# Kernel tuning notes

Hardware: AMD Instinct MI355X
Metric: run time of the kernel (lower is better)

## Reference

```python
import jax, jax.numpy as jnp
import numpy as np

H = 16          # n_heads
DN = 128        # qk_nope_head_dim
DR = 64         # qk_rope_head_dim
DV = 128        # v_head_dim
R = 512         # kv_lora_rank
DIM = 2048
THETA = 10000.0
EPS = 1e-6
SCALE = (DN + DR) ** -0.5


def rms_norm(x, w):
    var = jnp.mean(x * x, axis=-1, keepdims=True)
    return x * jax.lax.rsqrt(var + EPS) * w


def rope_cos_sin(seqlen):
    # DeepSeek freqs: 1/theta^(2i/d) over adjacent pairs
    inv = 1.0 / (THETA ** (jnp.arange(0, DR, 2, dtype=jnp.float32) / DR))  # [DR/2]
    ang = jnp.arange(seqlen, dtype=jnp.float32)[:, None] * inv             # [s, DR/2]
    return jnp.cos(ang), jnp.sin(ang)


def apply_rope(t, cos, sin):
    # t: [b, s, h, DR]; rotate adjacent pairs (complex multiply)
    b, s, h, d = t.shape
    t = t.reshape(b, s, h, d // 2, 2)
    x0, x1 = t[..., 0], t[..., 1]
    c = cos[None, :, None, :]
    sn = sin[None, :, None, :]
    out = jnp.stack([x0 * c - x1 * sn, x0 * sn + x1 * c], axis=-1)
    return out.reshape(b, s, h, d)


def setup_inputs() -> dict:
    key = jax.random.key(0)
    ks = jax.random.split(key, 6)
    b, s = 2, 2048
    sc = lambda n: n ** -0.5
    return {
        "x": jax.random.normal(ks[0], (b, s, DIM), jnp.float32),
        "wq": jax.random.normal(ks[1], (DIM, H * (DN + DR)), jnp.float32) * sc(DIM),
        "wkv_a": jax.random.normal(ks[2], (DIM, R + DR), jnp.float32) * sc(DIM),
        "kv_norm_w": jnp.ones((R,), jnp.float32),
        "wkv_b": jax.random.normal(ks[3], (R, H * (DN + DV)), jnp.float32) * sc(R),
        "wo": jax.random.normal(ks[4], (H * DV, DIM), jnp.float32) * sc(H * DV),
    }


def reference(x, wq, wkv_a, kv_norm_w, wkv_b, wo):
    b, s, _ = x.shape
    cos, sin = rope_cos_sin(s)

    # Query projection (q_lora_rank == 0 -> direct)
    q = (x @ wq).reshape(b, s, H, DN + DR)
    q_nope, q_pe = q[..., :DN], q[..., DN:]
    q_pe = apply_rope(q_pe, cos, sin)

    # Compressed KV + decoupled rope key
    kv_a = x @ wkv_a                      # [b, s, R+DR]
    kv, k_pe = kv_a[..., :R], kv_a[..., R:]
    k_pe = apply_rope(k_pe[:, :, None, :], cos, sin)  # [b, s, 1, DR]
    kv = rms_norm(kv, kv_norm_w)
    kvb = (kv @ wkv_b).reshape(b, s, H, DN + DV)
    k_nope, v = kvb[..., :DN], kvb[..., DN:]

    qf = jnp.concatenate([q_nope, q_pe], axis=-1)                         # [b,s,H,192]
    kf = jnp.concatenate([k_nope, jnp.broadcast_to(k_pe, (b, s, H, DR))], axis=-1)

    scores = jnp.einsum("bshd,bthd->bhst", qf, kf) * SCALE
    mask = jnp.tril(jnp.ones((s, s), bool))
    scores = jnp.where(mask[None, None], scores, jnp.finfo(scores.dtype).min)
    p = jax.nn.softmax(scores, axis=-1)
    out = jnp.einsum("bhst,bthd->bshd", p, v).reshape(b, s, H * DV)
    return out @ wo
```

## Files before the change

kernel.cpp:

```cpp
#include <hip/hip_runtime.h>
#include <hip/hip_bf16.h>
#include <math.h>

#define NB 2
#define NS 2048
#define ND 2048
#define NH 16
#define DNOPE 128
#define DROPE 64
#define DVAL 128
#define RANK 512
#define QW (NH*(DNOPE+DROPE))
#define AW (RANK+DROPE)
#define AWPAD 640
#define BW (NH*(DNOPE+DVAL))
#define OW (NH*DVAL)
#define ATT_SCALE2 0.10411758590510176f
#define LOG2_10000 13.287712379549449f

typedef __attribute__((ext_vector_type(8))) short short8;
typedef __attribute__((ext_vector_type(4))) float f32x4;

__device__ __forceinline__ float b2f(unsigned short u) {
  unsigned x = ((unsigned)u) << 16; float f; __builtin_memcpy(&f, &x, 4); return f;
}
__device__ __forceinline__ unsigned short f2b(float f) {
  unsigned x; __builtin_memcpy(&x, &f, 4);
  unsigned r = (x + 0x7fffu + ((x >> 16) & 1u)) >> 16;
  return (unsigned short)r;
}
__device__ __forceinline__ unsigned cvtpk(float a, float b) {
  unsigned r;
  asm("v_cvt_pk_bf16_f32 %0, %1, %2" : "=v"(r) : "v"(a), "v"(b));
  return r;
}
__device__ __forceinline__ void gload16(const void* g, void* lds) {
  __builtin_amdgcn_global_load_lds((const __attribute__((address_space(1))) void*)g,
                                   (__attribute__((address_space(3))) void*)lds, 16, 0, 0);
}

__global__ __launch_bounds__(256) void k_cvt(const float* __restrict__ X,
                                             unsigned short* __restrict__ Y) {
  long i = ((long)blockIdx.x * 256 + threadIdx.x) * 4;
  float4 v = *(const float4*)(X + i);
  ushort4 o;
  o.x = f2b(v.x); o.y = f2b(v.y); o.z = f2b(v.z); o.w = f2b(v.w);
  *(ushort4*)(Y + i) = o;
}

__global__ __launch_bounds__(256) void k_transpose(const float* __restrict__ W,
                                                   unsigned short* __restrict__ WT,
                                                   int K, int N) {
  __shared__ float t[32][33];
  const int k0 = blockIdx.x * 32, n0 = blockIdx.y * 32;
  const int tx = threadIdx.x & 31, ty = threadIdx.x >> 5;
  #pragma unroll
  for (int i = 0; i < 32; i += 8) {
    int n = n0 + tx;
    float v = (n < N) ? W[(size_t)(k0 + ty + i) * N + n] : 0.f;
    t[ty + i][tx] = v;
  }
  __syncthreads();
  #pragma unroll
  for (int i = 0; i < 32; i += 8)
    WT[(size_t)(n0 + ty + i) * K + k0 + tx] = f2b(t[tx][ty + i]);
}

template <typename OutT>
__global__ __launch_bounds__(256) void gemm_bf16(
    const unsigned short* __restrict__ A, const unsigned short* __restrict__ BT,
    OutT* __restrict__ C, int M, int N, int K, int lda) {
  __shared__ short8 AsV[1024];
  __shared__ short8 BsV[1024];
  const int tid = threadIdx.x;
  const int l = tid & 63, w = tid >> 6;
  const int nwg = gridDim.x * gridDim.y;
  const int bid = blockIdx.y * gridDim.x + blockIdx.x;
  const int sbid = (bid & 7) * (nwg >> 3) + (bid >> 3);
  const int bx = sbid % gridDim.x, by = sbid / gridDim.x;
  const int bm = by * 128, bn = bx * 128;
  const int wm = (w >> 1) * 64, wn = (w & 1) * 64;
  f32x4 acc[4][4] = {};

  const int srow = tid >> 3;
  const int gk   = ((((tid & 7) * 16) ^ ((srow & 7) << 4)) >> 1);
  const int sw   = l & 7;

  for (int k0 = 0; k0 < K; k0 += 64) {
    #pragma unroll
    for (int i = 0; i < 4; ++i) {
      const int row = i * 32 + srow;
      gload16(A + (size_t)(bm + row) * lda + k0 + gk, (char*)AsV + i * 4096 + w * 1024);
      gload16(BT + (size_t)(bn + row) * K   + k0 + gk, (char*)BsV + i * 4096 + w * 1024);
    }
    __syncthreads();
    #pragma unroll
    for (int kk2 = 0; kk2 < 2; ++kk2) {
      const int kb = kk2 * 4 + (l >> 4);
      short8 af[4], bg[4];
      #pragma unroll
      for (int mi = 0; mi < 4; ++mi)
        af[mi] = AsV[(wm + mi * 16 + (l & 15)) * 8 + (kb ^ sw)];
      #pragma unroll
      for (int ni = 0; ni < 4; ++ni)
        bg[ni] = BsV[(wn + ni * 16 + (l & 15)) * 8 + (kb ^ sw)];
      #pragma unroll
      for (int mi = 0; mi < 4; ++mi)
        #pragma unroll
        for (int ni = 0; ni < 4; ++ni)
          acc[mi][ni] = __builtin_amdgcn_mfma_f32_16x16x32_bf16(af[mi], bg[ni], acc[mi][ni], 0, 0, 0);
    }
    __syncthreads();
  }

  const int r0 = bm + wm + (l >> 4) * 4;
  const int c0 = bn + wn + (l & 15);
  #pragma unroll
  for (int mi = 0; mi < 4; ++mi)
    #pragma unroll
    for (int ni = 0; ni < 4; ++ni) {
      const int col = c0 + ni * 16;
      if (col < N) {
        #pragma unroll
        for (int j = 0; j < 4; ++j) {
          float v = acc[mi][ni][j];
          if constexpr (__is_same(OutT, float))
            C[(size_t)(r0 + mi * 16 + j) * N + col] = v;
          else
            C[(size_t)(r0 + mi * 16 + j) * N + col] = f2b(v);
        }
      }
    }
}

__global__ __launch_bounds__(256) void gemm_fused_qkva(
    const unsigned short* __restrict__ A, const unsigned short* __restrict__ BT,
    unsigned short* __restrict__ Cq, unsigned short* __restrict__ Ckva, int K) {
  __shared__ short8 AsV[1024];
  __shared__ short8 BsV[1024];
  const int tid = threadIdx.x;
  const int l = tid & 63, w = tid >> 6;
  const int nwg = gridDim.x * gridDim.y;
  const int bid = blockIdx.y * gridDim.x + blockIdx.x;
  const int sbid = (bid & 7) * (nwg >> 3) + (bid >> 3);
  const int bx = sbid % gridDim.x, by = sbid / gridDim.x;
  const int bm = by * 128, bn = bx * 128;
  const int wm = (w >> 1) * 64, wn = (w & 1) * 64;
  f32x4 acc[4][4] = {};

  const int srow = tid >> 3;
  const int gk   = ((((tid & 7) * 16) ^ ((srow & 7) << 4)) >> 1);
  const int sw   = l & 7;

  for (int k0 = 0; k0 < K; k0 += 64) {
    #pragma unroll
    for (int i = 0; i < 4; ++i) {
      const int row = i * 32 + srow;
      gload16(A + (size_t)(bm + row) * K + k0 + gk, (char*)AsV + i * 4096 + w * 1024);
      gload16(BT + (size_t)(bn + row) * K + k0 + gk, (char*)BsV + i * 4096 + w * 1024);
    }
    __syncthreads();
    #pragma unroll
    for (int kk2 = 0; kk2 < 2; ++kk2) {
      const int kb = kk2 * 4 + (l >> 4);
      short8 af[4], bg[4];
      #pragma unroll
      for (int mi = 0; mi < 4; ++mi)
        af[mi] = AsV[(wm + mi * 16 + (l & 15)) * 8 + (kb ^ sw)];
      #pragma unroll
      for (int ni = 0; ni < 4; ++ni)
        bg[ni] = BsV[(wn + ni * 16 + (l & 15)) * 8 + (kb ^ sw)];
      #pragma unroll
      for (int mi = 0; mi < 4; ++mi)
        #pragma unroll
        for (int ni = 0; ni < 4; ++ni)
          acc[mi][ni] = __builtin_amdgcn_mfma_f32_16x16x32_bf16(af[mi], bg[ni], acc[mi][ni], 0, 0, 0);
    }
    __syncthreads();
  }

  const int r0 = bm + wm + (l >> 4) * 4;
  const int c0 = bn + wn + (l & 15);
  #pragma unroll
  for (int mi = 0; mi < 4; ++mi)
    #pragma unroll
    for (int ni = 0; ni < 4; ++ni) {
      const int col = c0 + ni * 16;
      #pragma unroll
      for (int j = 0; j < 4; ++j) {
        const float v = acc[mi][ni][j];
        const int row = r0 + mi * 16 + j;
        if (col < QW)
          Cq[(size_t)row * QW + col] = f2b(v);
        else if (col - QW < AW)
          Ckva[(size_t)row * AW + (col - QW)] = f2b(v);
      }
    }
}

__global__ __launch_bounds__(256) void k_rms_b(unsigned short* __restrict__ kva,
                                               const float* __restrict__ w) {
  const int row = blockIdx.x;
  unsigned short* p = kva + (long)row * AW;
  __shared__ float sd[256];
  float ss = 0.f;
  for (int j = threadIdx.x; j < RANK; j += 256) { float v = b2f(p[j]); ss += v * v; }
  sd[threadIdx.x] = ss;
  __syncthreads();
  for (int st = 128; st > 0; st >>= 1) {
    if (threadIdx.x < st) sd[threadIdx.x] += sd[threadIdx.x + st];
    __syncthreads();
  }
  const float sc = rsqrtf(sd[0] / (float)RANK + 1e-6f);
  for (int j = threadIdx.x; j < RANK; j += 256) p[j] = f2b(b2f(p[j]) * sc * w[j]);
}

__global__ __launch_bounds__(64) void k_ropek_b(unsigned short* __restrict__ kva) {
  const int row = blockIdx.x;
  const int t = row & (NS - 1);
  const int i = threadIdx.x;
  if (i >= 32) return;
  const float invf = exp2f(-(float)i * (LOG2_10000 / 32.0f));
  const float ang = (float)t * invf;
  float s, c;
  sincosf(ang, &s, &c);
  unsigned short* p = kva + (long)row * AW + RANK + 2 * i;
  const float x0 = b2f(p[0]), x1 = b2f(p[1]);
  p[0] = f2b(x0 * c - x1 * s);
  p[1] = f2b(x0 * s + x1 * c);
}

__global__ __launch_bounds__(512) void k_ropeq_b(unsigned short* __restrict__ q) {
  const int row = blockIdx.x;
  const int t = row & (NS - 1);
  const int h = threadIdx.x >> 5;
  const int i = threadIdx.x & 31;
  const float invf = exp2f(-(float)i * (LOG2_10000 / 32.0f));
  const float ang = (float)t * invf;
  float s, c;
  sincosf(ang, &s, &c);
  unsigned short* p = q + (long)row * QW + h * (DNOPE + DROPE) + DNOPE + 2 * i;
  const float x0 = b2f(p[0]), x1 = b2f(p[1]);
  p[0] = f2b(x0 * c - x1 * s);
  p[1] = f2b(x0 * s + x1 * c);
}

#define KBLK 64
#define KSL 24
#define VTS 72
#define VBUF (DVAL*VTS)
#define PLS 72
#define QTILES (NS/128)
__global__ __launch_bounds__(512) void k_attn_mfma(
    const unsigned short* __restrict__ qg,
    const unsigned short* __restrict__ kvbg,
    const unsigned short* __restrict__ kvag,
    unsigned short* __restrict__ attg) {
  __shared__ short8 Ks[KBLK * KSL];
  __shared__ __align__(16) unsigned short VT[2 * VBUF];
  __shared__ __align__(16) unsigned short Pl[128 * PLS];
  const int tid = threadIdx.x;
  const int l = tid & 63, w = tid >> 6;
  const int g = l >> 4, r16 = l & 15;
  const int h = blockIdx.y;
  const int b = blockIdx.z;
  const int qt = b ? (QTILES - 1 - (int)blockIdx.x) : (int)blockIdx.x;
  const int nt = 2 * qt + 2;
  const int qrow0 = qt * 128 + w * 16;
  const unsigned short* q   = qg   + (size_t)b * NS * QW;
  const unsigned short* kvb = kvbg + (size_t)b * NS * BW;
  const unsigned short* kva = kvag + (size_t)b * NS * AW;
  unsigned short* att = attg + (size_t)b * NS * OW;

  const unsigned short* kbs[3]; int kstp[3]; char* kdst[3];
  #pragma unroll
  for (int i = 0; i < 3; ++i) {
    const int chunk = i * 512 + tid;
    const int row = chunk / KSL, p = chunk % KSL;
    const int s = (p & ~7) | ((p & 7) ^ (row & 7));
    const int d0 = s * 8;
    if (d0 < DNOPE) { kbs[i] = kvb + (size_t)row * BW + h * 256 + d0; kstp[i] = KBLK * BW; }
    else            { kbs[i] = kva + (size_t)row * AW + RANK + (d0 - DNOPE); kstp[i] = KBLK * AW; }
    kdst[i] = (char*)Ks + (size_t)(i * 512 + (tid & ~63)) * 16;
  }
  const int vt_t = tid >> 3, vqd = tid & 7;
  const unsigned short* vbs = kvb + (size_t)vt_t * BW + h * 256 + DNOPE + vqd * 8;
  unsigned short* vwd = VT + (vqd * 8) * VTS + (vt_t ^ (vqd << 3));

  short8 aq[6];
  {
    const unsigned short* qp = q + (size_t)(qrow0 + r16) * QW + h * 192 + g * 8;
    #pragma unroll
    for (int f = 0; f < 6; ++f) aq[f] = *(const short8*)(qp + f * 32);
  }
  f32x4 o[8] = {};
  float m_j[4], l_j[4];
  #pragma unroll
  for (int j = 0; j < 4; ++j) { m_j[j] = -1e30f; l_j[j] = 0.f; }

  const unsigned short* kq0 = kbs[0];
  const unsigned short* kq1 = kbs[1];
  const unsigned short* kq2 = kbs[2];
  const unsigned short* vq  = vbs;

  gload16(kq0, kdst[0]); kq0 += kstp[0];
  gload16(kq1, kdst[1]); kq1 += kstp[1];
  gload16(kq2, kdst[2]); kq2 += kstp[2];
  {
    short8 vA = *(const short8*)(vq);
    short8 vB = *(const short8*)(vq + 64);
    #pragma unroll
    for (int jj = 0; jj < 8; ++jj) {
      vwd[jj * VTS] = (unsigned short)vA[jj];
      vwd[64 * VTS + jj * VTS] = (unsigned short)vB[jj];
    }
    vq += KBLK * BW;
  }
  __syncthreads();
  int cur = 0;

  for (int kt = 0; kt < nt; ++kt) {
    f32x4 sa[4] = {};
    __builtin_amdgcn_s_setprio(1);
    #pragma unroll
    for (int f = 0; f < 6; ++f) {
      #pragma unroll
      for (int n = 0; n < 4; ++n) {
        const int row = n * 16 + r16;
        const int s = f * 4 + g;
        const int phys = (s & ~7) | ((s & 7) ^ (row & 7));
        short8 bg = Ks[row * KSL + phys];
        sa[n] = __builtin_amdgcn_mfma_f32_16x16x32_bf16(aq[f], bg, sa[n], 0, 0, 0);
      }
    }
    __builtin_amdgcn_s_setprio(0);
    __syncthreads();

    const bool pref = (kt + 1 < nt);
    short8 vA, vB;
    if (pref) {
      gload16(kq0, kdst[0]); kq0 += kstp[0];
      gload16(kq1, kdst[1]); kq1 += kstp[1];
      gload16(kq2, kdst[2]); kq2 += kstp[2];
      vA = *(const short8*)(vq);
      vB = *(const short8*)(vq + 64);
      vq += KBLK * BW;
    }

    const bool diag = (kt >= nt - 2);
    float pj[4][4];
    #pragma unroll
    for (int n = 0; n < 4; ++n) {
      const int key = kt * KBLK + n * 16 + r16;
      #pragma unroll
      for (int j = 0; j < 4; ++j) {
        float v = sa[n][j] * ATT_SCALE2;
        if (diag && key > (qrow0 + g * 4 + j)) v = -1e30f;
        pj[n][j] = v;
      }
    }
    float mjl[4];
    #pragma unroll
    for (int j = 0; j < 4; ++j)
      mjl[j] = fmaxf(fmaxf(pj[0][j], pj[1][j]), fmaxf(pj[2][j], pj[3][j]));
    const bool myneed = (mjl[0] > m_j[0] + 8.f) | (mjl[1] > m_j[1] + 8.f) |
                        (mjl[2] > m_j[2] + 8.f) | (mjl[3] > m_j[3] + 8.f);
    if (__any(myneed)) {
      #pragma unroll
      for (int j = 0; j < 4; ++j) {
        float mx = mjl[j];
        #pragma unroll
        for (int o2 = 1; o2 < 16; o2 <<= 1) mx = fmaxf(mx, __shfl_xor(mx, o2, 64));
        const float mn = fmaxf(m_j[j], mx);
        const float c = exp2f(m_j[j] - mn);
        l_j[j] *= c;
        #pragma unroll
        for (int n8 = 0; n8 < 8; ++n8) o[n8][j] *= c;
        m_j[j] = mn;
      }
    }
    #pragma unroll
    for (int j = 0; j < 4; ++j) {
      float p0 = exp2f(pj[0][j] - m_j[j]);
      float p1 = exp2f(pj[1][j] - m_j[j]);
      float p2 = exp2f(pj[2][j] - m_j[j]);
      float p3 = exp2f(pj[3][j] - m_j[j]);
      l_j[j] += (p0 + p1) + (p2 + p3);
      const int prow = w * 16 + g * 4 + j;
      const unsigned pk01 = cvtpk(p0, p1);
      const unsigned pk23 = cvtpk(p2, p3);
      Pl[prow * PLS +  0 + r16] = (unsigned short)pk01;
      Pl[prow * PLS + 16 + r16] = (unsigned short)(pk01 >> 16);
      Pl[prow * PLS + 32 + r16] = (unsigned short)pk23;
      Pl[prow * PLS + 48 + r16] = (unsigned short)(pk23 >> 16);
    }

    if (pref) {
      unsigned short* dst = vwd + (cur ^ 1) * VBUF;
      #pragma unroll
      for (int jj = 0; jj < 8; ++jj) {
        dst[jj * VTS] = (unsigned short)vA[jj];
        dst[64 * VTS + jj * VTS] = (unsigned short)vB[jj];
      }
    }

    const int hb = r16 >> 3;
    const unsigned short* vbase = VT + cur * VBUF;
    #pragma unroll
    for (int kk = 0; kk < 2; ++kk) {
      short8 pa = *(const short8*)&Pl[(w * 16 + r16) * PLS + kk * 32 + g * 8];
      __builtin_amdgcn_s_setprio(1);
      #pragma unroll
      for (int n8 = 0; n8 < 8; ++n8) {
        const int blk = (kk * 4 + g) ^ ((n8 * 2 + hb) & 7);
        short8 vb = *(const short8*)&vbase[(n8 * 16 + r16) * VTS + blk * 8];
        o[n8] = __builtin_amdgcn_mfma_f32_16x16x32_bf16(pa, vb, o[n8], 0, 0, 0);
      }
      __builtin_amdgcn_s_setprio(0);
    }
    __syncthreads();
    cur ^= 1;
  }

  #pragma unroll
  for (int j = 0; j < 4; ++j) {
    float ls = l_j[j];
    #pragma unroll
    for (int o2 = 1; o2 < 16; o2 <<= 1) ls += __shfl_xor(ls, o2, 64);
    const float inv = 1.0f / ls;
    const size_t rowoff = (size_t)(qrow0 + g * 4 + j) * OW + h * DVAL;
    #pragma unroll
    for (int n8 = 0; n8 < 8; ++n8)
      att[rowoff + n8 * 16 + r16] = f2b(o[n8][j] * inv);
  }
}

extern "C" void kernel_launch(void* const* d_in, const int* in_sizes, int n_in,
                              void* d_out, int out_size, void* d_ws, size_t ws_size,
                              hipStream_t stream) {
  const float* x      = (const float*)d_in[0];
  const float* wq     = (const float*)d_in[1];
  const float* wkv_a  = (const float*)d_in[2];
  const float* w_norm = (const float*)d_in[3];
  const float* wkv_b  = (const float*)d_in[4];
  const float* wo     = (const float*)d_in[5];
  float* out = (float*)d_out;

  unsigned short* wqT   = (unsigned short*)d_ws;
  unsigned short* wkvaT = wqT   + (long)QW * ND;
  unsigned short* wkvbT = wkvaT + (long)AWPAD * ND;
  unsigned short* woT   = wkvbT + (long)BW * RANK;
  unsigned short* xb2   = woT   + (long)ND * OW;
  unsigned short* q2    = xb2   + (long)NB * NS * ND;
  unsigned short* kva2  = q2    + (long)NB * NS * QW;
  unsigned short* kvb2  = kva2  + (long)NB * NS * AW;
  unsigned short* att2  = xb2;

  k_transpose<<<dim3(ND / 32, QW / 32),    dim3(256), 0, stream>>>(wq,    wqT,   ND,  QW);
  k_transpose<<<dim3(ND / 32, AWPAD / 32), dim3(256), 0, stream>>>(wkv_a, wkvaT, ND,  AW);
  k_transpose<<<dim3(RANK / 32, BW / 32),  dim3(256), 0, stream>>>(wkv_b, wkvbT, RANK, BW);
  k_transpose<<<dim3(OW / 32, ND / 32),    dim3(256), 0, stream>>>(wo,    woT,   OW,  ND);

  k_cvt<<<dim3((NB * NS * ND) / 1024), dim3(256), 0, stream>>>(x, xb2);
  gemm_fused_qkva<<<dim3((QW + AWPAD) / 128, (NB * NS) / 128), dim3(256), 0, stream>>>(
      xb2, wqT, q2, kva2, ND);
  k_rms_b<<<dim3(NB * NS), dim3(256), 0, stream>>>(kva2, w_norm);
  k_ropek_b<<<dim3(NB * NS), dim3(64), 0, stream>>>(kva2);
  k_ropeq_b<<<dim3(NB * NS), dim3(512), 0, stream>>>(q2);
  gemm_bf16<unsigned short><<<dim3(BW / 128, (NB * NS) / 128), dim3(256), 0, stream>>>(
      kva2, wkvbT, kvb2, NB * NS, BW, RANK, AW);
  k_attn_mfma<<<dim3(QTILES, NH, NB), dim3(512), 0, stream>>>(q2, kvb2, kva2, att2);
  gemm_bf16<float><<<dim3(ND / 128, (NB * NS) / 128), dim3(256), 0, stream>>>(
      att2, woT, out, NB * NS, ND, OW, OW);
}
```

Baseline: 333.1 us.

## Fuse RMS norm with key RoPE and pair causal query tiles per attention block

Merges the kv RMS-norm and key RoPE kernels into one 64-thread kernel that uses a vectorised load and a wavefront shuffle reduction, removing one launch and the shared-memory tree reduction. The attention kernel now processes two query tiles per block (tile i and its mirror QTILES-1-i) sequentially, with the grid halved. This balances causal work so every block does the same number of key tiles, at the cost of half as many blocks and a longer serial run per block, which may reduce occupancy and latency hiding.

```diff
diff --git a/kernel.cpp b/kernel.cpp
--- a/kernel.cpp
+++ b/kernel.cpp
@@ -198,36 +198,40 @@
     }
 }
 
-__global__ __launch_bounds__(256) void k_rms_b(unsigned short* __restrict__ kva,
-                                               const float* __restrict__ w) {
-  const int row = blockIdx.x;
-  unsigned short* p = kva + (long)row * AW;
-  __shared__ float sd[256];
-  float ss = 0.f;
-  for (int j = threadIdx.x; j < RANK; j += 256) { float v = b2f(p[j]); ss += v * v; }
-  sd[threadIdx.x] = ss;
-  __syncthreads();
-  for (int st = 128; st > 0; st >>= 1) {
-    if (threadIdx.x < st) sd[threadIdx.x] += sd[threadIdx.x + st];
-    __syncthreads();
-  }
-  const float sc = rsqrtf(sd[0] / (float)RANK + 1e-6f);
-  for (int j = threadIdx.x; j < RANK; j += 256) p[j] = f2b(b2f(p[j]) * sc * w[j]);
-}
-
-__global__ __launch_bounds__(64) void k_ropek_b(unsigned short* __restrict__ kva) {
+__global__ __launch_bounds__(64) void k_rms_ropek(unsigned short* __restrict__ kva,
+                                                  const float* __restrict__ w) {
   const int row = blockIdx.x;
   const int t = row & (NS - 1);
-  const int i = threadIdx.x;
-  if (i >= 32) return;
-  const float invf = exp2f(-(float)i * (LOG2_10000 / 32.0f));
-  const float ang = (float)t * invf;
-  float s, c;
-  sincosf(ang, &s, &c);
-  unsigned short* p = kva + (long)row * AW + RANK + 2 * i;
-  const float x0 = b2f(p[0]), x1 = b2f(p[1]);
-  p[0] = f2b(x0 * c - x1 * s);
-  p[1] = f2b(x0 * s + x1 * c);
+  const int lane = threadIdx.x;
+  unsigned short* p = kva + (long)row * AW;
+
+  short8 v = *(const short8*)(p + lane * 8);
+  float f[8];
+  float ss = 0.f;
+  #pragma unroll
+  for (int j = 0; j < 8; ++j) {
+    f[j] = b2f((unsigned short)v[j]);
+    ss += f[j] * f[j];
+  }
+  #pragma unroll
+  for (int o2 = 1; o2 < 64; o2 <<= 1) ss += __shfl_xor(ss, o2, 64);
+  const float sc = rsqrtf(ss / (float)RANK + 1e-6f);
+  short8 ov;
+  #pragma unroll
+  for (int j = 0; j < 8; ++j)
+    ov[j] = (short)f2b(f[j] * sc * w[lane * 8 + j]);
+  *(short8*)(p + lane * 8) = ov;
+
+  if (lane < 32) {
+    const float invf = exp2f(-(float)lane * (LOG2_10000 / 32.0f));
+    const float ang = (float)t * invf;
+    float s, c;
+    sincosf(ang, &s, &c);
+    unsigned short* pp = p + RANK + 2 * lane;
+    const float x0 = b2f(pp[0]), x1 = b2f(pp[1]);
+    pp[0] = f2b(x0 * c - x1 * s);
+    pp[1] = f2b(x0 * s + x1 * c);
+  }
 }
 
 __global__ __launch_bounds__(512) void k_ropeq_b(unsigned short* __restrict__ q) {
@@ -264,9 +268,6 @@
   const int g = l >> 4, r16 = l & 15;
   const int h = blockIdx.y;
   const int b = blockIdx.z;
-  const int qt = b ? (QTILES - 1 - (int)blockIdx.x) : (int)blockIdx.x;
-  const int nt = 2 * qt + 2;
-  const int qrow0 = qt * 128 + w * 16;
   const unsigned short* q   = qg   + (size_t)b * NS * QW;
   const unsigned short* kvb = kvbg + (size_t)b * NS * BW;
   const unsigned short* kva = kvag + (size_t)b * NS * AW;
@@ -287,151 +288,159 @@
   const unsigned short* vbs = kvb + (size_t)vt_t * BW + h * 256 + DNOPE + vqd * 8;
   unsigned short* vwd = VT + (vqd * 8) * VTS + (vt_t ^ (vqd << 3));
 
-  short8 aq[6];
-  {
-    const unsigned short* qp = q + (size_t)(qrow0 + r16) * QW + h * 192 + g * 8;
-    #pragma unroll
-    for (int f = 0; f < 6; ++f) aq[f] = *(const short8*)(qp + f * 32);
-  }
-  f32x4 o[8] = {};
-  float m_j[4], l_j[4];
-  #pragma unroll
-  for (int j = 0; j < 4; ++j) { m_j[j] = -1e30f; l_j[j] = 0.f; }
-
-  const unsigned short* kq0 = kbs[0];
-  const unsigned short* kq1 = kbs[1];
-  const unsigned short* kq2 = kbs[2];
-  const unsigned short* vq  = vbs;
-
-  gload16(kq0, kdst[0]); kq0 += kstp[0];
-  gload16(kq1, kdst[1]); kq1 += kstp[1];
-  gload16(kq2, kdst[2]); kq2 += kstp[2];
-  {
-    short8 vA = *(const short8*)(vq);
-    short8 vB = *(const short8*)(vq + 64);
-    #pragma unroll
-    for (int jj = 0; jj < 8; ++jj) {
-      vwd[jj * VTS] = (unsigned short)vA[jj];
-      vwd[64 * VTS + jj * VTS] = (unsigned short)vB[jj];
-    }
-    vq += KBLK * BW;
-  }
-  __syncthreads();
-  int cur = 0;
-
-  for (int kt = 0; kt < nt; ++kt) {
-    f32x4 sa[4] = {};
-    __builtin_amdgcn_s_setprio(1);
-    #pragma unroll
-    for (int f = 0; f < 6; ++f) {
+  #pragma unroll 1
+  for (int phase = 0; phase < 2; ++phase) {
+    const int qt = phase ? (QTILES - 1 - (int)blockIdx.x) : (int)blockIdx.x;
+    const int nt = 2 * qt + 2;
+    const int qrow0 = qt * 128 + w * 16;
+
+    short8 aq[6];
+    {
+      const unsigned short* qp = q + (size_t)(qrow0 + r16) * QW + h * 192 + g * 8;
+      #pragma unroll
+      for (int f = 0; f < 6; ++f) aq[f] = *(const short8*)(qp + f * 32);
+    }
+    f32x4 o[8] = {};
+    float m_j[4], l_j[4];
+    #pragma unroll
+    for (int j = 0; j < 4; ++j) { m_j[j] = -1e30f; l_j[j] = 0.f; }
+
+    const unsigned short* kq0 = kbs[0];
+    const unsigned short* kq1 = kbs[1];
+    const unsigned short* kq2 = kbs[2];
+    const unsigned short* vq  = vbs;
+
+    gload16(kq0, kdst[0]); kq0 += kstp[0];
+    gload16(kq1, kdst[1]); kq1 += kstp[1];
+    gload16(kq2, kdst[2]); kq2 += kstp[2];
+    {
+      short8 vA = *(const short8*)(vq);
+      short8 vB = *(const short8*)(vq + 64);
+      #pragma unroll
+      for (int jj = 0; jj < 8; ++jj) {
+        vwd[jj * VTS] = (unsigned short)vA[jj];
+        vwd[64 * VTS + jj * VTS] = (unsigned short)vB[jj];
+      }
+      vq += KBLK * BW;
+    }
+    __syncthreads();
+    int cur = 0;
+
+    for (int kt = 0; kt < nt; ++kt) {
+      f32x4 sa[4] = {};
+      __builtin_amdgcn_s_setprio(1);
+      #pragma unroll
+      for (int f = 0; f < 6; ++f) {
+        #pragma unroll
+        for (int n = 0; n < 4; ++n) {
+          const int row = n * 16 + r16;
+          const int s = f * 4 + g;
+          const int phys = (s & ~7) | ((s & 7) ^ (row & 7));
+          short8 bg = Ks[row * KSL + phys];
+          sa[n] = __builtin_amdgcn_mfma_f32_16x16x32_bf16(aq[f], bg, sa[n], 0, 0, 0);
+        }
+      }
+      __builtin_amdgcn_s_setprio(0);
+      __syncthreads();
+
+      const bool pref = (kt + 1 < nt);
+      short8 vA, vB;
+      if (pref) {
+        gload16(kq0, kdst[0]); kq0 += kstp[0];
+        gload16(kq1, kdst[1]); kq1 += kstp[1];
+        gload16(kq2, kdst[2]); kq2 += kstp[2];
+        vA = *(const short8*)(vq);
+        vB = *(const short8*)(vq + 64);
+        vq += KBLK * BW;
+      }
+
+      const bool diag = (kt >= nt - 2);
+      float pj[4][4];
       #pragma unroll
       for (int n = 0; n < 4; ++n) {
-        const int row = n * 16 + r16;
-        const int s = f * 4 + g;
-        const int phys = (s & ~7) | ((s & 7) ^ (row & 7));
-        short8 bg = Ks[row * KSL + phys];
-        sa[n] = __builtin_amdgcn_mfma_f32_16x16x32_bf16(aq[f], bg, sa[n], 0, 0, 0);
-      }
-    }
-    __builtin_amdgcn_s_setprio(0);
-    __syncthreads();
-
-    const bool pref = (kt + 1 < nt);
-    short8 vA, vB;
-    if (pref) {
-      gload16(kq0, kdst[0]); kq0 += kstp[0];
-      gload16(kq1, kdst[1]); kq1 += kstp[1];
-      gload16(kq2, kdst[2]); kq2 += kstp[2];
-      vA = *(const short8*)(vq);
-      vB = *(const short8*)(vq + 64);
-      vq += KBLK * BW;
-    }
-
-    const bool diag = (kt >= nt - 2);
-    float pj[4][4];
-    #pragma unroll
-    for (int n = 0; n < 4; ++n) {
-      const int key = kt * KBLK + n * 16 + r16;
+        const int key = kt * KBLK + n * 16 + r16;
+        #pragma unroll
+        for (int j = 0; j < 4; ++j) {
+          float v = sa[n][j] * ATT_SCALE2;
+          if (diag && key > (qrow0 + g * 4 + j)) v = -1e30f;
+          pj[n][j] = v;
+        }
+      }
+      float mjl[4];
+      #pragma unroll
+      for (int j = 0; j < 4; ++j)
+        mjl[j] = fmaxf(fmaxf(pj[0][j], pj[1][j]), fmaxf(pj[2][j], pj[3][j]));
+      const bool myneed = (mjl[0] > m_j[0] + 8.f) | (mjl[1] > m_j[1] + 8.f) |
+                          (mjl[2] > m_j[2] + 8.f) | (mjl[3] > m_j[3] + 8.f);
+      if (__any(myneed)) {
+        #pragma unroll
+        for (int j = 0; j < 4; ++j) {
+          float mx = mjl[j];
+          #pragma unroll
+          for (int o2 = 1; o2 < 16; o2 <<= 1) mx = fmaxf(mx, __shfl_xor(mx, o2, 64));
+          const float mn = fmaxf(m_j[j], mx);
+          const float c = exp2f(m_j[j] - mn);
+          l_j[j] *= c;
+          #pragma unroll
+          for (int n8 = 0; n8 < 8; ++n8) o[n8][j] *= c;
+          m_j[j] = mn;
+        }
+      }
       #pragma unroll
       for (int j = 0; j < 4; ++j) {
-        float v = sa[n][j] * ATT_SCALE2;
-        if (diag && key > (qrow0 + g * 4 + j)) v = -1e30f;
-        pj[n][j] = v;
-      }
-    }
-    float mjl[4];
-    #pragma unroll
-    for (int j = 0; j < 4; ++j)
-      mjl[j] = fmaxf(fmaxf(pj[0][j], pj[1][j]), fmaxf(pj[2][j], pj[3][j]));
-    const bool myneed = (mjl[0] > m_j[0] + 8.f) | (mjl[1] > m_j[1] + 8.f) |
-                        (mjl[2] > m_j[2] + 8.f) | (mjl[3] > m_j[3] + 8.f);
-    if (__any(myneed)) {
-      #pragma unroll
-      for (int j = 0; j < 4; ++j) {
-        float mx = mjl[j];
-        #pragma unroll
-        for (int o2 = 1; o2 < 16; o2 <<= 1) mx = fmaxf(mx, __shfl_xor(mx, o2, 64));
-        const float mn = fmaxf(m_j[j], mx);
-        const float c = exp2f(m_j[j] - mn);
-        l_j[j] *= c;
-        #pragma unroll
-        for (int n8 = 0; n8 < 8; ++n8) o[n8][j] *= c;
-        m_j[j] = mn;
-      }
-    }
+        float p0 = exp2f(pj[0][j] - m_j[j]);
+        float p1 = exp2f(pj[1][j] - m_j[j]);
+        float p2 = exp2f(pj[2][j] - m_j[j]);
+        float p3 = exp2f(pj[3][j] - m_j[j]);
+        l_j[j] += (p0 + p1) + (p2 + p3);
+        const int prow = w * 16 + g * 4 + j;
+        const unsigned pk01 = cvtpk(p0, p1);
+        const unsigned pk23 = cvtpk(p2, p3);
+        Pl[prow * PLS +  0 + r16] = (unsigned short)pk01;
+        Pl[prow * PLS + 16 + r16] = (unsigned short)(pk01 >> 16);
+        Pl[prow * PLS + 32 + r16] = (unsigned short)pk23;
+        Pl[prow * PLS + 48 + r16] = (unsigned short)(pk23 >> 16);
+      }
+
+      if (pref) {
+        unsigned short* dst = vwd + (cur ^ 1) * VBUF;
+        #pragma unroll
+        for (int jj = 0; jj < 8; ++jj) {
+          dst[jj * VTS] = (unsigned short)vA[jj];
+          dst[64 * VTS + jj * VTS] = (unsigned short)vB[jj];
+        }
+      }
+
+      const int hb = r16 >> 3;
+      const unsigned short* vbase = VT + cur * VBUF;
+      #pragma unroll
+      for (int kk = 0; kk < 2; ++kk) {
+        short8 pa = *(const short8*)&Pl[(w * 16 + r16) * PLS + kk * 32 + g * 8];
+        __builtin_amdgcn_s_setprio(1);
+        #pragma unroll
+        for (int n8 = 0; n8 < 8; ++n8) {
+          const int blk = (kk * 4 + g) ^ ((n8 * 2 + hb) & 7);
+          short8 vb = *(const short8*)&vbase[(n8 * 16 + r16) * VTS + blk * 8];
+          o[n8] = __builtin_amdgcn_mfma_f32_16x16x32_bf16(pa, vb, o[n8], 0, 0, 0);
+        }
+        __builtin_amdgcn_s_setprio(0);
+      }
+      __syncthreads();
+      cur ^= 1;
+    }
+
     #pragma unroll
     for (int j = 0; j < 4; ++j) {
-      float p0 = exp2f(pj[0][j] - m_j[j]);
-      float p1 = exp2f(pj[1][j] - m_j[j]);
-      float p2 = exp2f(pj[2][j] - m_j[j]);
-      float p3 = exp2f(pj[3][j] - m_j[j]);
-      l_j[j] += (p0 + p1) + (p2 + p3);
-      const int prow = w * 16 + g * 4 + j;
-      const unsigned pk01 = cvtpk(p0, p1);
-      const unsigned pk23 = cvtpk(p2, p3);
-      Pl[prow * PLS +  0 + r16] = (unsigned short)pk01;
-      Pl[prow * PLS + 16 + r16] = (unsigned short)(pk01 >> 16);
-      Pl[prow * PLS + 32 + r16] = (unsigned short)pk23;
-      Pl[prow * PLS + 48 + r16] = (unsigned short)(pk23 >> 16);
-    }
-
-    if (pref) {
-      unsigned short* dst = vwd + (cur ^ 1) * VBUF;
-      #pragma unroll
-      for (int jj = 0; jj < 8; ++jj) {
-        dst[jj * VTS] = (unsigned short)vA[jj];
-        dst[64 * VTS + jj * VTS] = (unsigned short)vB[jj];
-      }
-    }
-
-    const int hb = r16 >> 3;
-    const unsigned short* vbase = VT + cur * VBUF;
-    #pragma unroll
-    for (int kk = 0; kk < 2; ++kk) {
-      short8 pa = *(const short8*)&Pl[(w * 16 + r16) * PLS + kk * 32 + g * 8];
-      __builtin_amdgcn_s_setprio(1);
-      #pragma unroll
-      for (int n8 = 0; n8 < 8; ++n8) {
-        const int blk = (kk * 4 + g) ^ ((n8 * 2 + hb) & 7);
-        short8 vb = *(const short8*)&vbase[(n8 * 16 + r16) * VTS + blk * 8];
-        o[n8] = __builtin_amdgcn_mfma_f32_16x16x32_bf16(pa, vb, o[n8], 0, 0, 0);
-      }
-      __builtin_amdgcn_s_setprio(0);
-    }
-    __syncthreads();
-    cur ^= 1;
-  }
-
-  #pragma unroll
-  for (int j = 0; j < 4; ++j) {
-    float ls = l_j[j];
-    #pragma unroll
-    for (int o2 = 1; o2 < 16; o2 <<= 1) ls += __shfl_xor(ls, o2, 64);
-    const float inv = 1.0f / ls;
-    const size_t rowoff = (size_t)(qrow0 + g * 4 + j) * OW + h * DVAL;
-    #pragma unroll
-    for (int n8 = 0; n8 < 8; ++n8)
-      att[rowoff + n8 * 16 + r16] = f2b(o[n8][j] * inv);
+      float ls = l_j[j];
+      #pragma unroll
+      for (int o2 = 1; o2 < 16; o2 <<= 1) ls += __shfl_xor(ls, o2, 64);
+      const float inv = 1.0f / ls;
+      const size_t rowoff = (size_t)(qrow0 + g * 4 + j) * OW + h * DVAL;
+      #pragma unroll
+      for (int n8 = 0; n8 < 8; ++n8)
+        att[rowoff + n8 * 16 + r16] = f2b(o[n8][j] * inv);
+    }
+    __syncthreads();
   }
 }
 
@@ -464,12 +473,11 @@
   k_cvt<<<dim3((NB * NS * ND) / 1024), dim3(256), 0, stream>>>(x, xb2);
   gemm_fused_qkva<<<dim3((QW + AWPAD) / 128, (NB * NS) / 128), dim3(256), 0, stream>>>(
       xb2, wqT, q2, kva2, ND);
-  k_rms_b<<<dim3(NB * NS), dim3(256), 0, stream>>>(kva2, w_norm);
-  k_ropek_b<<<dim3(NB * NS), dim3(64), 0, stream>>>(kva2);
+  k_rms_ropek<<<dim3(NB * NS), dim3(64), 0, stream>>>(kva2, w_norm);
   k_ropeq_b<<<dim3(NB * NS), dim3(512), 0, stream>>>(q2);
   gemm_bf16<unsigned short><<<dim3(BW / 128, (NB * NS) / 128), dim3(256), 0, stream>>>(
       kva2, wkvbT, kvb2, NB * NS, BW, RANK, AW);
-  k_attn_mfma<<<dim3(QTILES, NH, NB), dim3(512), 0, stream>>>(q2, kvb2, kva2, att2);
+  k_attn_mfma<<<dim3(QTILES / 2, NH, NB), dim3(512), 0, stream>>>(q2, kvb2, kva2, att2);
   gemm_bf16<float><<<dim3(ND / 128, (NB * NS) / 128), dim3(256), 0, stream>>>(
       att2, woT, out, NB * NS, ND, OW, OW);
 }
```

After: 293.8 us. 11.8% less time.
